# Optimization experiments

Hardware: AMD Instinct MI355X
Metric: run time of the kernel (lower is better)

The kernel has to match this reference:

```python
import jax, jax.numpy as jnp
import numpy as np

NUM_EXPERTS = 8
TOP_K = 2


def setup_inputs() -> dict:
    key = jax.random.key(0)
    ks = jax.random.split(key, 5)
    B, S, D, F, E = 4, 2048, 1024, 4096, NUM_EXPERTS
    scale = 0.02
    x = jax.random.normal(ks[0], (B, S, D), dtype=jnp.float32)
    W_gate = jax.random.normal(ks[1], (E, D), dtype=jnp.float32) * scale  # router: logits = x @ W_gate.T
    Wg = jax.random.normal(ks[2], (E, F, D), dtype=jnp.float32) * scale   # per-expert gate_proj
    Wu = jax.random.normal(ks[3], (E, F, D), dtype=jnp.float32) * scale   # per-expert up_proj
    Wd = jax.random.normal(ks[4], (E, D, F), dtype=jnp.float32) * scale   # per-expert down_proj
    return {"x": x, "W_gate": W_gate, "Wg": Wg, "Wu": Wu, "Wd": Wd}


def reference(x, W_gate, Wg, Wu, Wd):
    # Router: softmax over experts, then top-k, renormalize.
    gate_logits = jnp.einsum('bsd,ed->bse', x, W_gate)
    probs = jax.nn.softmax(gate_logits, axis=-1)
    top_w, top_i = jax.lax.top_k(probs, TOP_K)                # (B,S,K)
    top_w = top_w / jnp.sum(top_w, axis=-1, keepdims=True)

    output = jnp.zeros_like(x)
    for e in range(NUM_EXPERTS):
        # combined routing weight for expert e (0 for tokens not routed to e)
        w_e = jnp.sum(jnp.where(top_i == e, top_w, 0.0), axis=-1)  # (B,S)
        gate = jax.nn.silu(jnp.einsum('bsd,fd->bsf', x, Wg[e]))
        up = jnp.einsum('bsd,fd->bsf', x, Wu[e])
        out_e = jnp.einsum('bsf,df->bsd', gate * up, Wd[e])
        output = output + out_e * w_e[..., None]
    return output
```

## Files before the change

kernel.cpp:

```cpp
#include <hip/hip_runtime.h>
#include <hip/hip_bf16.h>

#define T_TOK 8192
#define D_DIM 1024
#define F_DIM 4096
#define NE 8

#define BM 128
#define BK 32

typedef _Float16 v8h __attribute__((ext_vector_type(8)));
typedef float f32x4 __attribute__((ext_vector_type(4)));

__device__ __forceinline__ void async_lds16(void* lds, const void* g) {
    __builtin_amdgcn_global_load_lds(
        (const __attribute__((address_space(1))) void*)g,
        (__attribute__((address_space(3))) void*)lds,
        16, 0, 0);
}

__global__ void router_kernel(const float* __restrict__ x,
                              const float* __restrict__ Wgate,
                              int* __restrict__ cnt,
                              int* __restrict__ rows,
                              float* __restrict__ wts) {
    int t = blockIdx.x;
    int lane = threadIdx.x;
    const float* xr = x + (size_t)t * D_DIM;
    float acc[NE];
#pragma unroll
    for (int e = 0; e < NE; ++e) acc[e] = 0.f;
#pragma unroll
    for (int i = 0; i < D_DIM / 64; ++i) {
        int d = i * 64 + lane;
        float xv = xr[d];
#pragma unroll
        for (int e = 0; e < NE; ++e) acc[e] += xv * Wgate[e * D_DIM + d];
    }
#pragma unroll
    for (int off = 32; off > 0; off >>= 1) {
#pragma unroll
        for (int e = 0; e < NE; ++e) acc[e] += __shfl_xor(acc[e], off, 64);
    }
    if (lane == 0) {
        int e0 = 0;
#pragma unroll
        for (int e = 1; e < NE; ++e) if (acc[e] > acc[e0]) e0 = e;
        int e1 = (e0 == 0) ? 1 : 0;
#pragma unroll
        for (int e = 0; e < NE; ++e) if (e != e0 && acc[e] > acc[e1]) e1 = e;
        float w0 = 1.f / (1.f + __expf(acc[e1] - acc[e0]));
        float w1 = 1.f - w0;
        int p0 = atomicAdd(&cnt[e0], 1);
        rows[e0 * T_TOK + p0] = 2 * t;
        wts[e0 * T_TOK + p0] = w0;
        int p1 = atomicAdd(&cnt[e1], 1);
        rows[e1 * T_TOK + p1] = 2 * t + 1;
        wts[e1 * T_TOK + p1] = w1;
    }
}

__global__ void f32to16_kernel(const float* __restrict__ src, _Float16* __restrict__ dst) {
    int i = blockIdx.x * blockDim.x + threadIdx.x;
    float4 v = ((const float4*)src)[i];
    union { _Float16 h[4]; uint2 u; } pk;
    pk.h[0] = (_Float16)v.x; pk.h[1] = (_Float16)v.y;
    pk.h[2] = (_Float16)v.z; pk.h[3] = (_Float16)v.w;
    *(uint2*)&dst[(size_t)i * 4] = pk.u;
}

__global__ __launch_bounds__(256, 2)
void gateup_kernel(const _Float16* __restrict__ Xh,
                   const _Float16* __restrict__ Wgh,
                   const _Float16* __restrict__ Wuh,
                   const int* __restrict__ cnt,
                   const int* __restrict__ rows,
                   const float* __restrict__ wts,
                   _Float16* __restrict__ H) {
    int e = blockIdx.z;
    int c = cnt[e];
    int row0 = blockIdx.y * BM;
    if (row0 >= c) return;
    int col0 = blockIdx.x * 64;

    __shared__ __align__(16) char smem[128 * 66 * 4];
    _Float16 (*As)[BK] = (_Float16(*)[BK])smem;
    _Float16 (*Bs)[BK] = (_Float16(*)[BK])(smem + BM * BK * 2);
    float (*ex)[66] = (float(*)[66])smem;
    __shared__ int hrow_s[BM];
    __shared__ float w_s[BM];

    int tid = threadIdx.x;
    int lane = tid & 63;
    int wave = tid >> 6;
    int wr = wave >> 1, wc = wave & 1;

    if (tid < BM) {
        int p = row0 + tid;
        if (p < c) { hrow_s[tid] = rows[e * T_TOK + p]; w_s[tid] = wts[e * T_TOK + p]; }
        else       { hrow_s[tid] = -1;                  w_s[tid] = 0.f; }
    }
    __syncthreads();

    int srow = tid >> 2;
    int kch = tid & 3;
    int hr0 = hrow_s[srow], hr1 = hrow_s[srow + 64];
    int tok0 = (hr0 >= 0) ? (hr0 >> 1) : 0;
    int tok1 = (hr1 >= 0) ? (hr1 >> 1) : 0;

    const _Float16* a0 = Xh + (size_t)tok0 * D_DIM + kch * 8;
    const _Float16* a1 = Xh + (size_t)tok1 * D_DIM + kch * 8;
    const _Float16* bg = Wgh + ((size_t)e * F_DIM + col0 + srow) * D_DIM + kch * 8;
    const _Float16* bu = Wuh + ((size_t)e * F_DIM + col0 + srow) * D_DIM + kch * 8;

    _Float16* lA0 = &As[srow][kch * 8];
    _Float16* lA1 = &As[srow + 64][kch * 8];
    _Float16* lB0 = &Bs[srow][kch * 8];
    _Float16* lB1 = &Bs[srow + 64][kch * 8];

    f32x4 acc[4][4];
#pragma unroll
    for (int i = 0; i < 4; ++i)
#pragma unroll
        for (int j = 0; j < 4; ++j) acc[i][j] = (f32x4)0.f;

    int m16 = lane & 15, q8 = (lane >> 4) * 8;

    for (int k0 = 0; k0 < D_DIM; k0 += BK) {
        async_lds16(lA0, a0 + k0);
        async_lds16(lA1, a1 + k0);
        async_lds16(lB0, bg + k0);
        async_lds16(lB1, bu + k0);
        __syncthreads();

        v8h af[4], bf[4];
#pragma unroll
        for (int i = 0; i < 4; ++i)
            af[i] = *(const v8h*)&As[wr * 64 + i * 16 + m16][q8];
#pragma unroll
        for (int j = 0; j < 4; ++j)
            bf[j] = *(const v8h*)&Bs[wc * 64 + j * 16 + m16][q8];
#pragma unroll
        for (int i = 0; i < 4; ++i)
#pragma unroll
            for (int j = 0; j < 4; ++j)
                acc[i][j] = __builtin_amdgcn_mfma_f32_16x16x32_f16(af[i], bf[j], acc[i][j], 0, 0, 0);
        __syncthreads();
    }

    int q = lane >> 4, cl = lane & 15;
    if (wc == 0) {
#pragma unroll
        for (int i = 0; i < 4; ++i)
#pragma unroll
            for (int r4 = 0; r4 < 4; ++r4) {
                int r = wr * 64 + i * 16 + q * 4 + r4;
                float w = w_s[r];
#pragma unroll
                for (int j = 0; j < 4; ++j) {
                    float g = acc[i][j][r4];
                    ex[r][j * 16 + cl] = g / (1.f + __expf(-g)) * w;
                }
            }
    }
    __syncthreads();
    if (wc == 1) {
#pragma unroll
        for (int i = 0; i < 4; ++i)
#pragma unroll
            for (int r4 = 0; r4 < 4; ++r4) {
                int r = wr * 64 + i * 16 + q * 4 + r4;
                int hr = hrow_s[r];
                if (hr < 0) continue;
#pragma unroll
                for (int j = 0; j < 4; ++j) {
                    float h = ex[r][j * 16 + cl] * acc[i][j][r4];
                    H[(size_t)hr * F_DIM + col0 + j * 16 + cl] = (_Float16)h;
                }
            }
    }
}

__global__ __launch_bounds__(256, 2)
void down_kernel(const _Float16* __restrict__ H,
                 const _Float16* __restrict__ Wdh,
                 const int* __restrict__ cnt,
                 const int* __restrict__ rows,
                 float* __restrict__ O) {
    int e = blockIdx.z;
    int c = cnt[e];
    int row0 = blockIdx.y * BM;
    if (row0 >= c) return;
    int col0 = blockIdx.x * 128;

    __shared__ __align__(16) _Float16 As[BM][BK];
    __shared__ __align__(16) _Float16 Bs[128][BK];
    __shared__ int hrow_s[BM];

    int tid = threadIdx.x;
    int lane = tid & 63;
    int wave = tid >> 6;
    int wr = wave >> 1, wc = wave & 1;

    if (tid < BM) {
        int p = row0 + tid;
        hrow_s[tid] = (p < c) ? rows[e * T_TOK + p] : -1;
    }
    __syncthreads();

    int srow = tid >> 2;
    int kch = tid & 3;
    int hr0 = hrow_s[srow], hr1 = hrow_s[srow + 64];
    int r0 = (hr0 >= 0) ? hr0 : 0;
    int r1 = (hr1 >= 0) ? hr1 : 0;

    const _Float16* a0 = H + (size_t)r0 * F_DIM + kch * 8;
    const _Float16* a1 = H + (size_t)r1 * F_DIM + kch * 8;
    const _Float16* b0 = Wdh + ((size_t)e * D_DIM + col0 + srow) * F_DIM + kch * 8;
    const _Float16* b1 = b0 + (size_t)64 * F_DIM;

    _Float16* lA0 = &As[srow][kch * 8];
    _Float16* lA1 = &As[srow + 64][kch * 8];
    _Float16* lB0 = &Bs[srow][kch * 8];
    _Float16* lB1 = &Bs[srow + 64][kch * 8];

    f32x4 acc[4][4];
#pragma unroll
    for (int i = 0; i < 4; ++i)
#pragma unroll
        for (int j = 0; j < 4; ++j) acc[i][j] = (f32x4)0.f;

    int m16 = lane & 15, q8 = (lane >> 4) * 8;

    for (int k0 = 0; k0 < F_DIM; k0 += BK) {
        async_lds16(lA0, a0 + k0);
        async_lds16(lA1, a1 + k0);
        async_lds16(lB0, b0 + k0);
        async_lds16(lB1, b1 + k0);
        __syncthreads();

        v8h af[4], bf[4];
#pragma unroll
        for (int i = 0; i < 4; ++i)
            af[i] = *(const v8h*)&As[wr * 64 + i * 16 + m16][q8];
#pragma unroll
        for (int j = 0; j < 4; ++j)
            bf[j] = *(const v8h*)&Bs[wc * 64 + j * 16 + m16][q8];
#pragma unroll
        for (int i = 0; i < 4; ++i)
#pragma unroll
            for (int j = 0; j < 4; ++j)
                acc[i][j] = __builtin_amdgcn_mfma_f32_16x16x32_f16(af[i], bf[j], acc[i][j], 0, 0, 0);
        __syncthreads();
    }

    int q = lane >> 4, cl = lane & 15;
#pragma unroll
    for (int i = 0; i < 4; ++i) {
#pragma unroll
        for (int r4 = 0; r4 < 4; ++r4) {
            int r = wr * 64 + i * 16 + q * 4 + r4;
            int hr = hrow_s[r];
            if (hr < 0) continue;
#pragma unroll
            for (int j = 0; j < 4; ++j) {
                int col = col0 + wc * 64 + j * 16 + cl;
                O[(size_t)hr * D_DIM + col] = acc[i][j][r4];
            }
        }
    }
}

__global__ void combine_kernel(const float* __restrict__ O, float* __restrict__ out) {
    int t = blockIdx.x;
    int d = threadIdx.x;
    const float4* a = (const float4*)(O + (size_t)(2 * t) * D_DIM);
    const float4* b = (const float4*)(O + (size_t)(2 * t + 1) * D_DIM);
    float4 va = a[d], vb = b[d];
    float4 r; r.x = va.x + vb.x; r.y = va.y + vb.y; r.z = va.z + vb.z; r.w = va.w + vb.w;
    ((float4*)(out + (size_t)t * D_DIM))[d] = r;
}

extern "C" void kernel_launch(void* const* d_in, const int* in_sizes, int n_in,
                              void* d_out, int out_size, void* d_ws, size_t ws_size,
                              hipStream_t stream) {
    const float* x     = (const float*)d_in[0];
    const float* Wgate = (const float*)d_in[1];
    const float* Wg    = (const float*)d_in[2];
    const float* Wu    = (const float*)d_in[3];
    const float* Wd    = (const float*)d_in[4];
    float* out = (float*)d_out;

    char* w = (char*)d_ws;
    int*      cnt  = (int*)w;
    int*      rows = (int*)(w + 1024);
    float*    wts  = (float*)(w + 263168);
    _Float16* Xh   = (_Float16*)(w + 525312);

    const size_t OFF_WGH = 17302528;
    const size_t OFF_WUH = 84411392;
    const size_t OFF_WDH = 151520256;
    const size_t OFF_H   = 218629120;
    const size_t OFF_O   = 352846848;

    _Float16* Wgh = (_Float16*)(w + OFF_WGH);
    _Float16* Wuh = (_Float16*)(w + OFF_WUH);
    _Float16* Wdh = (_Float16*)(w + OFF_WDH);
    _Float16* H   = (_Float16*)(w + OFF_H);
    float*    O   = (float*)(w + OFF_O);

    hipMemsetAsync(w, 0, 1024, stream);

    router_kernel<<<T_TOK, 64, 0, stream>>>(x, Wgate, cnt, rows, wts);
    f32to16_kernel<<<(T_TOK * D_DIM / 4) / 256, 256, 0, stream>>>(x, Xh);

    const int WN4 = (NE * F_DIM * D_DIM / 4);
    f32to16_kernel<<<WN4 / 256, 256, 0, stream>>>(Wg, Wgh);
    f32to16_kernel<<<WN4 / 256, 256, 0, stream>>>(Wu, Wuh);
    f32to16_kernel<<<WN4 / 256, 256, 0, stream>>>(Wd, Wdh);

    gateup_kernel<<<dim3(F_DIM / 64, T_TOK / BM, NE), 256, 0, stream>>>(
        Xh, Wgh, Wuh, cnt, rows, wts, H);
    down_kernel<<<dim3(D_DIM / 128, T_TOK / BM, NE), 256, 0, stream>>>(
        H, Wdh, cnt, rows, O);
    combine_kernel<<<T_TOK, 256, 0, stream>>>(O, out);
}
```

Baseline: 1.236 ms.

## Rewrite gate/up GEMM with larger tiles, double-buffered LDS and swizzled layout

The gate/up expert GEMM moves to 256x128 tiles with BK=64, 512 threads, and separate gate and up accumulators per wave instead of splitting gate and up across wave columns. Global-to-LDS loads are double-buffered and interleaved with MFMA phases using partial vmcnt waits, barriers and s_setprio, and LDS reads use an XOR swizzle to avoid bank conflicts. The SiLU(gate)*up*weight epilogue is now computed in registers without the LDS exchange. The aim is more data reuse per byte loaded and hiding load latency behind matrix math. In exchange, register and LDS use rise, and padding waste grows for experts whose token count is not a multiple of 256.

Result: slower. 1.289 ms (+4.3%).

```diff
diff --git a/kernel.cpp b/kernel.cpp
--- a/kernel.cpp
+++ b/kernel.cpp
@@ -8,6 +8,11 @@
 
 #define BM 128
 #define BK 32
+
+#define BM2 256
+#define BN2 128
+#define BK2 64
+#define KT2 (D_DIM / BK2)
 
 typedef _Float16 v8h __attribute__((ext_vector_type(8)));
 typedef float f32x4 __attribute__((ext_vector_type(4)));
@@ -69,7 +74,7 @@
     *(uint2*)&dst[(size_t)i * 4] = pk.u;
 }
 
-__global__ __launch_bounds__(256, 2)
+__global__ __launch_bounds__(512, 2)
 void gateup_kernel(const _Float16* __restrict__ Xh,
                    const _Float16* __restrict__ Wgh,
                    const _Float16* __restrict__ Wuh,
@@ -79,105 +84,187 @@
                    _Float16* __restrict__ H) {
     int e = blockIdx.z;
     int c = cnt[e];
-    int row0 = blockIdx.y * BM;
+    int row0 = blockIdx.y * BM2;
     if (row0 >= c) return;
-    int col0 = blockIdx.x * 64;
-
-    __shared__ __align__(16) char smem[128 * 66 * 4];
-    _Float16 (*As)[BK] = (_Float16(*)[BK])smem;
-    _Float16 (*Bs)[BK] = (_Float16(*)[BK])(smem + BM * BK * 2);
-    float (*ex)[66] = (float(*)[66])smem;
-    __shared__ int hrow_s[BM];
-    __shared__ float w_s[BM];
+    int col0 = blockIdx.x * BN2;
+
+    __shared__ __align__(16) _Float16 Ab[2][BM2][BK2];
+    __shared__ __align__(16) _Float16 Bb[2][BM2][BK2];
+    __shared__ int hrow_s[BM2];
+    __shared__ float w_s[BM2];
 
     int tid = threadIdx.x;
     int lane = tid & 63;
-    int wave = tid >> 6;
-    int wr = wave >> 1, wc = wave & 1;
-
-    if (tid < BM) {
+    int wv = tid >> 6;
+    int wr = wv >> 2;
+    int wc = wv & 3;
+
+    if (tid < BM2) {
         int p = row0 + tid;
         if (p < c) { hrow_s[tid] = rows[e * T_TOK + p]; w_s[tid] = wts[e * T_TOK + p]; }
         else       { hrow_s[tid] = -1;                  w_s[tid] = 0.f; }
     }
     __syncthreads();
 
-    int srow = tid >> 2;
-    int kch = tid & 3;
-    int hr0 = hrow_s[srow], hr1 = hrow_s[srow + 64];
-    int tok0 = (hr0 >= 0) ? (hr0 >> 1) : 0;
-    int tok1 = (hr1 >= 0) ? (hr1 >> 1) : 0;
-
-    const _Float16* a0 = Xh + (size_t)tok0 * D_DIM + kch * 8;
-    const _Float16* a1 = Xh + (size_t)tok1 * D_DIM + kch * 8;
-    const _Float16* bg = Wgh + ((size_t)e * F_DIM + col0 + srow) * D_DIM + kch * 8;
-    const _Float16* bu = Wuh + ((size_t)e * F_DIM + col0 + srow) * D_DIM + kch * 8;
-
-    _Float16* lA0 = &As[srow][kch * 8];
-    _Float16* lA1 = &As[srow + 64][kch * 8];
-    _Float16* lB0 = &Bs[srow][kch * 8];
-    _Float16* lB1 = &Bs[srow + 64][kch * 8];
-
-    f32x4 acc[4][4];
-#pragma unroll
-    for (int i = 0; i < 4; ++i)
-#pragma unroll
-        for (int j = 0; j < 4; ++j) acc[i][j] = (f32x4)0.f;
-
-    int m16 = lane & 15, q8 = (lane >> 4) * 8;
-
-    for (int k0 = 0; k0 < D_DIM; k0 += BK) {
-        async_lds16(lA0, a0 + k0);
-        async_lds16(lA1, a1 + k0);
-        async_lds16(lB0, bg + k0);
-        async_lds16(lB1, bu + k0);
-        __syncthreads();
-
-        v8h af[4], bf[4];
-#pragma unroll
-        for (int i = 0; i < 4; ++i)
-            af[i] = *(const v8h*)&As[wr * 64 + i * 16 + m16][q8];
-#pragma unroll
-        for (int j = 0; j < 4; ++j)
-            bf[j] = *(const v8h*)&Bs[wc * 64 + j * 16 + m16][q8];
-#pragma unroll
-        for (int i = 0; i < 4; ++i)
-#pragma unroll
-            for (int j = 0; j < 4; ++j)
-                acc[i][j] = __builtin_amdgcn_mfma_f32_16x16x32_f16(af[i], bf[j], acc[i][j], 0, 0, 0);
-        __syncthreads();
-    }
-
-    int q = lane >> 4, cl = lane & 15;
-    if (wc == 0) {
-#pragma unroll
-        for (int i = 0; i < 4; ++i)
+    int l8 = lane >> 3;
+    int g  = lane & 7;
+    int lg = g ^ l8;
+
+    int r0 = wv * 16 + l8;
+    int r1 = r0 + 8;
+
+    int hA00 = hrow_s[r0],       hA01 = hrow_s[r1];
+    int hA10 = hrow_s[128 + r0], hA11 = hrow_s[128 + r1];
+    const _Float16* sA00 = Xh + (size_t)(hA00 >= 0 ? (hA00 >> 1) : 0) * D_DIM + lg * 8;
+    const _Float16* sA01 = Xh + (size_t)(hA01 >= 0 ? (hA01 >> 1) : 0) * D_DIM + lg * 8;
+    const _Float16* sA10 = Xh + (size_t)(hA10 >= 0 ? (hA10 >> 1) : 0) * D_DIM + lg * 8;
+    const _Float16* sA11 = Xh + (size_t)(hA11 >= 0 ? (hA11 >> 1) : 0) * D_DIM + lg * 8;
+    const _Float16* sB00 = Wgh + ((size_t)e * F_DIM + col0 + r0) * D_DIM + lg * 8;
+    const _Float16* sB01 = Wgh + ((size_t)e * F_DIM + col0 + r1) * D_DIM + lg * 8;
+    const _Float16* sB10 = Wuh + ((size_t)e * F_DIM + col0 + r0) * D_DIM + lg * 8;
+    const _Float16* sB11 = Wuh + ((size_t)e * F_DIM + col0 + r1) * D_DIM + lg * 8;
+
+    int stO0 = wv * 2048 + lane * 16;
+
+    int m16 = lane & 15, q4 = lane >> 4;
+    int rx = m16 & 7;
+    int cb0 = ((q4 ^ rx) << 4);
+    int cb1 = (((4 + q4) ^ rx) << 4);
+    const char* arB = (const char*)Ab + (wr * 16 + m16) * 128;
+    const char* brB = (const char*)Bb + m16 * 128 + wc * 4096;
+
+    {
+        char* a0 = (char*)Ab + stO0;
+        char* b0 = (char*)Bb + stO0;
+        async_lds16(b0,                sB00);
+        async_lds16(b0 + 1024,         sB01);
+        async_lds16(a0,                sA00);
+        async_lds16(a0 + 1024,         sA01);
+        async_lds16(b0 + 16384,        sB10);
+        async_lds16(b0 + 16384 + 1024, sB11);
+        async_lds16(a0 + 16384,        sA10);
+        async_lds16(a0 + 16384 + 1024, sA11);
+        asm volatile("s_waitcnt vmcnt(4)" ::: "memory");
+        __builtin_amdgcn_s_barrier();
+    }
+
+    f32x4 accg[8][2], accu[8][2];
+#pragma unroll
+    for (int i = 0; i < 8; ++i)
+#pragma unroll
+        for (int j = 0; j < 2; ++j) { accg[i][j] = (f32x4)0.f; accu[i][j] = (f32x4)0.f; }
+
+    int cur = 0;
+#pragma unroll 1
+    for (int t = 0; t < KT2; ++t) {
+        int kn = (t + 1 < KT2) ? (t + 1) * BK2 : 0;
+        int nb = cur ^ 1;
+        const char* ar = arB + cur * 32768;
+        const char* br = brB + cur * 32768;
+        char* aD = (char*)Ab + nb * 32768 + stO0;
+        char* bD = (char*)Bb + nb * 32768 + stO0;
+
+        v8h af[4][2], bg[2][2], bu[2][2];
+
+#pragma unroll
+        for (int i = 0; i < 4; ++i) {
+            af[i][0] = *(const v8h*)(ar + i * 4096 + cb0);
+            af[i][1] = *(const v8h*)(ar + i * 4096 + cb1);
+        }
+#pragma unroll
+        for (int j = 0; j < 2; ++j) {
+            bg[j][0] = *(const v8h*)(br + j * 2048 + cb0);
+            bg[j][1] = *(const v8h*)(br + j * 2048 + cb1);
+        }
+        async_lds16(bD,        sB00 + kn);
+        async_lds16(bD + 1024, sB01 + kn);
+        __builtin_amdgcn_s_barrier();
+        __builtin_amdgcn_s_setprio(1);
+#pragma unroll
+        for (int i = 0; i < 4; ++i)
+#pragma unroll
+            for (int j = 0; j < 2; ++j) {
+                accg[i][j] = __builtin_amdgcn_mfma_f32_16x16x32_f16(af[i][0], bg[j][0], accg[i][j], 0, 0, 0);
+                accg[i][j] = __builtin_amdgcn_mfma_f32_16x16x32_f16(af[i][1], bg[j][1], accg[i][j], 0, 0, 0);
+            }
+        __builtin_amdgcn_s_setprio(0);
+        asm volatile("s_waitcnt vmcnt(4)" ::: "memory");
+        __builtin_amdgcn_s_barrier();
+
+#pragma unroll
+        for (int j = 0; j < 2; ++j) {
+            bu[j][0] = *(const v8h*)(br + 16384 + j * 2048 + cb0);
+            bu[j][1] = *(const v8h*)(br + 16384 + j * 2048 + cb1);
+        }
+        async_lds16(aD,        sA00 + kn);
+        async_lds16(aD + 1024, sA01 + kn);
+        __builtin_amdgcn_s_barrier();
+        __builtin_amdgcn_s_setprio(1);
+#pragma unroll
+        for (int i = 0; i < 4; ++i)
+#pragma unroll
+            for (int j = 0; j < 2; ++j) {
+                accu[i][j] = __builtin_amdgcn_mfma_f32_16x16x32_f16(af[i][0], bu[j][0], accu[i][j], 0, 0, 0);
+                accu[i][j] = __builtin_amdgcn_mfma_f32_16x16x32_f16(af[i][1], bu[j][1], accu[i][j], 0, 0, 0);
+            }
+        __builtin_amdgcn_s_setprio(0);
+        asm volatile("s_waitcnt vmcnt(4)" ::: "memory");
+        __builtin_amdgcn_s_barrier();
+
+#pragma unroll
+        for (int i = 0; i < 4; ++i) {
+            af[i][0] = *(const v8h*)(ar + (i + 4) * 4096 + cb0);
+            af[i][1] = *(const v8h*)(ar + (i + 4) * 4096 + cb1);
+        }
+        async_lds16(bD + 16384,        sB10 + kn);
+        async_lds16(bD + 16384 + 1024, sB11 + kn);
+        __builtin_amdgcn_s_barrier();
+        __builtin_amdgcn_s_setprio(1);
+#pragma unroll
+        for (int i = 0; i < 4; ++i)
+#pragma unroll
+            for (int j = 0; j < 2; ++j) {
+                accg[i + 4][j] = __builtin_amdgcn_mfma_f32_16x16x32_f16(af[i][0], bg[j][0], accg[i + 4][j], 0, 0, 0);
+                accg[i + 4][j] = __builtin_amdgcn_mfma_f32_16x16x32_f16(af[i][1], bg[j][1], accg[i + 4][j], 0, 0, 0);
+            }
+        __builtin_amdgcn_s_setprio(0);
+        __builtin_amdgcn_s_barrier();
+
+        async_lds16(aD + 16384,        sA10 + kn);
+        async_lds16(aD + 16384 + 1024, sA11 + kn);
+        __builtin_amdgcn_s_barrier();
+        __builtin_amdgcn_s_setprio(1);
+#pragma unroll
+        for (int i = 0; i < 4; ++i)
+#pragma unroll
+            for (int j = 0; j < 2; ++j) {
+                accu[i + 4][j] = __builtin_amdgcn_mfma_f32_16x16x32_f16(af[i][0], bu[j][0], accu[i + 4][j], 0, 0, 0);
+                accu[i + 4][j] = __builtin_amdgcn_mfma_f32_16x16x32_f16(af[i][1], bu[j][1], accu[i + 4][j], 0, 0, 0);
+            }
+        __builtin_amdgcn_s_setprio(0);
+        asm volatile("s_waitcnt vmcnt(4)" ::: "memory");
+        __builtin_amdgcn_s_barrier();
+
+        cur = nb;
+    }
+
+    int cl = lane & 15;
+#pragma unroll
+    for (int i = 0; i < 8; ++i) {
+#pragma unroll
+        for (int j = 0; j < 2; ++j) {
+            f32x4 gv = accg[i][j];
+            f32x4 uv = accu[i][j];
 #pragma unroll
             for (int r4 = 0; r4 < 4; ++r4) {
-                int r = wr * 64 + i * 16 + q * 4 + r4;
-                float w = w_s[r];
-#pragma unroll
-                for (int j = 0; j < 4; ++j) {
-                    float g = acc[i][j][r4];
-                    ex[r][j * 16 + cl] = g / (1.f + __expf(-g)) * w;
-                }
-            }
-    }
-    __syncthreads();
-    if (wc == 1) {
-#pragma unroll
-        for (int i = 0; i < 4; ++i)
-#pragma unroll
-            for (int r4 = 0; r4 < 4; ++r4) {
-                int r = wr * 64 + i * 16 + q * 4 + r4;
+                int r = i * 32 + wr * 16 + q4 * 4 + r4;
                 int hr = hrow_s[r];
                 if (hr < 0) continue;
-#pragma unroll
-                for (int j = 0; j < 4; ++j) {
-                    float h = ex[r][j * 16 + cl] * acc[i][j][r4];
-                    H[(size_t)hr * F_DIM + col0 + j * 16 + cl] = (_Float16)h;
-                }
-            }
+                float gg = gv[r4];
+                float h = gg / (1.f + __expf(-gg)) * w_s[r] * uv[r4];
+                H[(size_t)hr * F_DIM + col0 + (wc * 2 + j) * 16 + cl] = (_Float16)h;
+            }
+        }
     }
 }
 
@@ -319,7 +406,7 @@
     f32to16_kernel<<<WN4 / 256, 256, 0, stream>>>(Wu, Wuh);
     f32to16_kernel<<<WN4 / 256, 256, 0, stream>>>(Wd, Wdh);
 
-    gateup_kernel<<<dim3(F_DIM / 64, T_TOK / BM, NE), 256, 0, stream>>>(
+    gateup_kernel<<<dim3(F_DIM / BN2, T_TOK / BM2, NE), 512, 0, stream>>>(
         Xh, Wgh, Wuh, cnt, rows, wts, H);
     down_kernel<<<dim3(D_DIM / 128, T_TOK / BM, NE), 256, 0, stream>>>(
         H, Wdh, cnt, rows, O);
```
